# Optimization experiments

Measured on AMD Instinct MI355X. Metric: run time of the kernel, lower is better.

Reference implementation:

```python
import jax, jax.numpy as jnp
import numpy as np

C = 1024
H = 16
D = C // H  # head_dim = 64
FF = 4 * C


def setup_inputs() -> dict:
    key = jax.random.key(0)
    ks = jax.random.split(key, 10)
    s = lambda fan_in: 1.0 / np.sqrt(fan_in)
    return {
        "x": jax.random.normal(ks[0], (2, 2048, C), dtype=jnp.float32),
        "ln1_g": jnp.ones((C,), jnp.float32),
        "ln1_b": jnp.zeros((C,), jnp.float32),
        "w_qkv": jax.random.normal(ks[1], (C, 3 * C), jnp.float32) * s(C),
        "w_proj": jax.random.normal(ks[2], (C, C), jnp.float32) * s(C),
        "b_proj": jnp.zeros((C,), jnp.float32),
        "ln2_g": jnp.ones((C,), jnp.float32),
        "ln2_b": jnp.zeros((C,), jnp.float32),
        "w_fc1": jax.random.normal(ks[3], (C, FF), jnp.float32) * s(C),
        "b_fc1": jnp.zeros((FF,), jnp.float32),
        "w_fc2": jax.random.normal(ks[4], (FF, C), jnp.float32) * s(FF),
        "b_fc2": jnp.zeros((C,), jnp.float32),
    }


def _layernorm(x, g, b, eps=1e-5):
    mu = jnp.mean(x, axis=-1, keepdims=True)
    var = jnp.var(x, axis=-1, keepdims=True)
    return (x - mu) * jax.lax.rsqrt(var + eps) * g + b


def reference(x, ln1_g, ln1_b, w_qkv, w_proj, b_proj, ln2_g, ln2_b, w_fc1, b_fc1, w_fc2, b_fc2):
    B, N, _ = x.shape
    scale = D ** -0.5
    # --- attention sub-block (pre-LN) ---
    h = _layernorm(x, ln1_g, ln1_b)
    qkv = (h @ w_qkv).reshape(B, N, 3, H, D)
    q, k, v = jnp.moveaxis(qkv, 2, 0)          # each [B, N, H, D]
    attn = jnp.einsum("bnhd,bmhd->bhnm", q, k) * scale  # [B,H,N,N]
    attn = jax.nn.softmax(attn, axis=-1)
    o = jnp.einsum("bhnm,bmhd->bnhd", attn, v).reshape(B, N, C)
    x = x + o @ w_proj + b_proj
    # --- MLP sub-block (pre-LN) ---
    h = _layernorm(x, ln2_g, ln2_b)
    h = jax.nn.gelu(h @ w_fc1 + b_fc1, approximate=False)
    x = x + h @ w_fc2 + b_fc2
    return x
```

## Files before the change

kernel.cpp:

```cpp
#include <hip/hip_runtime.h>
#include <hip/hip_bf16.h>

typedef unsigned short u16;
typedef unsigned int u32;
typedef __attribute__((ext_vector_type(8))) short bf16x8;
typedef __attribute__((ext_vector_type(4))) float f32x4;
typedef __attribute__((ext_vector_type(4))) int   i32x4;
typedef __attribute__((ext_vector_type(4))) float fvec4;

__device__ inline u16 f2bf(float f) {
    union { float f; unsigned u; } v; v.f = f;
    unsigned r = v.u + 0x7fffu + ((v.u >> 16) & 1u);
    return (u16)(r >> 16);
}

__device__ inline f32x4 mfma16(bf16x8 a, bf16x8 b, f32x4 c) {
    return __builtin_amdgcn_mfma_f32_16x16x32_bf16(a, b, c, 0, 0, 0);
}

__device__ inline void gload16(const void* g, void* l) {
    __builtin_amdgcn_global_load_lds(
        (const __attribute__((address_space(1))) unsigned int*)g,
        (__attribute__((address_space(3))) unsigned int*)l, 16, 0, 0);
}

__global__ __launch_bounds__(256)
void transpose_all(const float* __restrict__ w0, u16* __restrict__ o0,
                   const float* __restrict__ w1, u16* __restrict__ o1,
                   const float* __restrict__ w2, u16* __restrict__ o2,
                   const float* __restrict__ w3, u16* __restrict__ o3) {
    __shared__ float tile[32][33];
    int b = blockIdx.x;
    const float* in; u16* out; int K, N, local;
    if (b < 3072)      { in = w0; out = o0; K = 1024; N = 3072; local = b; }
    else if (b < 4096) { in = w1; out = o1; K = 1024; N = 1024; local = b - 3072; }
    else if (b < 8192) { in = w2; out = o2; K = 1024; N = 4096; local = b - 4096; }
    else               { in = w3; out = o3; K = 4096; N = 1024; local = b - 8192; }
    const int nx = N >> 5;
    const int n0 = (local % nx) * 32, k0 = (local / nx) * 32;
    const int x = threadIdx.x & 31, y = threadIdx.x >> 5;
    for (int i = 0; i < 4; ++i)
        tile[y + i * 8][x] = in[(size_t)(k0 + y + i * 8) * N + n0 + x];
    __syncthreads();
    for (int i = 0; i < 4; ++i) {
        int r = y + i * 8;
        out[(size_t)(n0 + r) * K + k0 + x] = f2bf(tile[x][r]);
    }
}

__global__ __launch_bounds__(256)
void vtrans(const u16* __restrict__ qkv, u16* __restrict__ vT) {
    __shared__ u32 tl[64][33];
    const int t0 = blockIdx.x * 64, f0 = blockIdx.y * 64;
    const int a = threadIdx.x & 31, yy = threadIdx.x >> 5;
    for (int i = 0; i < 8; ++i) {
        int t = yy + i * 8;
        tl[t][a] = *(const u32*)(qkv + (size_t)(t0 + t) * 3072 + 2048 + f0 + a * 2);
    }
    __syncthreads();
    for (int i = 0; i < 8; ++i) {
        int f = yy + i * 8;
        u32 lo = tl[2 * a][f >> 1], hi = tl[2 * a + 1][f >> 1];
        u32 r = (f & 1) ? ((lo >> 16) | (hi & 0xffff0000u))
                        : ((lo & 0xffffu) | (hi << 16));
        *(u32*)(vT + (size_t)(f0 + f) * 4096 + t0 + 2 * a) = r;
    }
}

__global__ __launch_bounds__(256)
void ln_kernel(const float* __restrict__ x, const float* __restrict__ g,
               const float* __restrict__ bvec, u16* __restrict__ out) {
    __shared__ float red[2][4];
    const int row = blockIdx.x, tid = threadIdx.x;
    const float* xr = x + (size_t)row * 1024;
    fvec4 v = *(const fvec4*)(xr + tid * 4);
    float s  = v[0] + v[1] + v[2] + v[3];
    float s2 = v[0]*v[0] + v[1]*v[1] + v[2]*v[2] + v[3]*v[3];
    for (int off = 1; off < 64; off <<= 1) {
        s  += __shfl_xor(s,  off);
        s2 += __shfl_xor(s2, off);
    }
    const int w = tid >> 6;
    if ((tid & 63) == 0) { red[0][w] = s; red[1][w] = s2; }
    __syncthreads();
    s  = red[0][0] + red[0][1] + red[0][2] + red[0][3];
    s2 = red[1][0] + red[1][1] + red[1][2] + red[1][3];
    const float mu  = s * (1.0f / 1024.0f);
    const float var = s2 * (1.0f / 1024.0f) - mu * mu;
    const float rstd = rsqrtf(var + 1e-5f);
    fvec4 gv = *(const fvec4*)(g + tid * 4);
    fvec4 bv = *(const fvec4*)(bvec + tid * 4);
    u16 o4[4];
    for (int i = 0; i < 4; ++i)
        o4[i] = f2bf((v[i] - mu) * rstd * gv[i] + bv[i]);
    u32 lo = (u32)o4[0] | ((u32)o4[1] << 16);
    u32 hi = (u32)o4[2] | ((u32)o4[3] << 16);
    u32* dst = (u32*)(out + (size_t)row * 1024 + tid * 4);
    dst[0] = lo; dst[1] = hi;
}

template <int MODE, int WM, int WN, int MT, int NT, int NYP>
__global__ __launch_bounds__(256)
void gemm64(const u16* __restrict__ A, const u16* __restrict__ Bt,
            const float* __restrict__ bias, const float* __restrict__ res,
            void* __restrict__ out, int M, int N, int K) {
    constexpr int TM = WM * MT * 16;
    constexpr int TN = WN * NT * 16;
    constexpr int AJ = TM / 64;
    constexpr int BJ = TN / 64;
    static_assert(TM == 128, "swizzle assumes 32 M-tiles");
    __shared__ __attribute__((aligned(16))) u16 sA[2 * TM * 32];
    __shared__ __attribute__((aligned(16))) u16 sB[2 * TN * 32];
    const int id = blockIdx.x;
    const int j  = id >> 3;
    const int by = (id & 7) * NYP + (j >> 5);
    const int bx = j & 31;
    const int tid = threadIdx.x;
    const int lane = tid & 63, w = tid >> 6;
    const int wm = w / WN, wn = w % WN;
    const int q = lane >> 4, l16 = lane & 15;

    f32x4 acc[MT][NT];
#pragma unroll
    for (int i = 0; i < MT; ++i)
#pragma unroll
        for (int jj = 0; jj < NT; ++jj) acc[i][jj] = (f32x4)0.0f;

    const int sr = lane >> 2;
    const int kc = (lane & 3) * 8;
    const u16* gA[AJ];
    const u16* gB[BJ];
#pragma unroll
    for (int jj = 0; jj < AJ; ++jj)
        gA[jj] = A + (size_t)(bx * TM + (jj * 4 + w) * 16 + sr) * K + kc;
#pragma unroll
    for (int jj = 0; jj < BJ; ++jj)
        gB[jj] = Bt + (size_t)(by * TN + (jj * 4 + w) * 16 + sr) * K + kc;

    for (int k0 = 0; k0 < K; k0 += 64) {
#pragma unroll
        for (int kt = 0; kt < 2; ++kt) {
#pragma unroll
            for (int jj = 0; jj < AJ; ++jj)
                gload16(gA[jj] + k0 + kt * 32, &sA[kt * TM * 32 + (jj * 4 + w) * 512]);
#pragma unroll
            for (int jj = 0; jj < BJ; ++jj)
                gload16(gB[jj] + k0 + kt * 32, &sB[kt * TN * 32 + (jj * 4 + w) * 512]);
        }
        __syncthreads();
#pragma unroll
        for (int kt = 0; kt < 2; ++kt) {
            bf16x8 af[MT], bf[NT];
#pragma unroll
            for (int mt = 0; mt < MT; ++mt)
                af[mt] = *(const bf16x8*)&sA[kt * TM * 32 +
                         (wm * MT * 16 + mt * 16 + l16) * 32 + q * 8];
#pragma unroll
            for (int nt = 0; nt < NT; ++nt)
                bf[nt] = *(const bf16x8*)&sB[kt * TN * 32 +
                         (wn * NT * 16 + nt * 16 + l16) * 32 + q * 8];
#pragma unroll
            for (int mt = 0; mt < MT; ++mt)
#pragma unroll
                for (int nt = 0; nt < NT; ++nt)
                    acc[mt][nt] = mfma16(af[mt], bf[nt], acc[mt][nt]);
        }
        __syncthreads();
    }

#pragma unroll
    for (int mt = 0; mt < MT; ++mt)
#pragma unroll
        for (int nt = 0; nt < NT; ++nt)
#pragma unroll
            for (int r = 0; r < 4; ++r) {
                const int row = bx * TM + wm * MT * 16 + mt * 16 + q * 4 + r;
                const int col = by * TN + wn * NT * 16 + nt * 16 + l16;
                const size_t idx = (size_t)row * N + col;
                float v = acc[mt][nt][r];
                if (MODE == 0) {
                    ((u16*)out)[idx] = f2bf(v);
                } else if (MODE == 1) {
                    ((float*)out)[idx] = v + bias[col] + res[idx];
                } else {
                    float t = v + bias[col];
                    ((u16*)out)[idx] = f2bf(t * 0.5f * (1.0f + erff(t * 0.70710678118f)));
                }
            }
}

__global__ __launch_bounds__(256)
void attention3(const u16* __restrict__ qkv, const u16* __restrict__ vT,
                u16* __restrict__ o) {
    __shared__ __attribute__((aligned(16))) u16 sK[64][72];
    __shared__ __attribute__((aligned(16))) u16 sV[64][72];

    const int tid = threadIdx.x;
    const int lane = tid & 63, w = tid >> 6;
    const int qc = lane >> 4, l16 = lane & 15;
    const int bx = blockIdx.x;
    const int qt = bx & 15, h = (bx >> 4) & 15, b = bx >> 8;
    const int rowbase = qt * 128 + w * 32;

    bf16x8 aQ[2][2];
#pragma unroll
    for (int mtq = 0; mtq < 2; ++mtq)
#pragma unroll
        for (int kd = 0; kd < 2; ++kd)
            aQ[mtq][kd] = *(const bf16x8*)(qkv +
                (size_t)(b * 2048 + rowbase + mtq * 16 + l16) * 3072 +
                h * 64 + kd * 32 + qc * 8);

    f32x4 accO[2][4];
#pragma unroll
    for (int mtq = 0; mtq < 2; ++mtq)
#pragma unroll
        for (int dt = 0; dt < 4; ++dt) accO[mtq][dt] = (f32x4)0.0f;
    float lsum[2] = {0.0f, 0.0f};

    const int srr = tid >> 3;
    const int sc8 = (tid & 7) * 8;
    const u16* gK = qkv + (size_t)(b * 2048 + srr) * 3072 + 1024 + h * 64 + sc8;
    const u16* gV = vT + (size_t)(h * 64 + srr) * 4096 + b * 2048 + sc8;

    i32x4 cK[2], cV[2];
    cK[0] = *(const i32x4*)gK;
    cK[1] = *(const i32x4*)(gK + (size_t)32 * 3072);
    cV[0] = *(const i32x4*)gV;
    cV[1] = *(const i32x4*)(gV + (size_t)32 * 4096);

    const int sig_base = ((l16 >> 2) << 3) + (l16 & 3);

    for (int kc = 0; kc < 32; ++kc) {
        __syncthreads();
        *(i32x4*)&sK[srr][sc8]      = cK[0];
        *(i32x4*)&sK[srr + 32][sc8] = cK[1];
        *(i32x4*)&sV[srr][sc8]      = cV[0];
        *(i32x4*)&sV[srr + 32][sc8] = cV[1];
        const int kn = (kc + 1 < 32) ? kc + 1 : 31;
        i32x4 nK[2], nV[2];
        nK[0] = *(const i32x4*)(gK + (size_t)kn * 64 * 3072);
        nK[1] = *(const i32x4*)(gK + ((size_t)kn * 64 + 32) * 3072);
        nV[0] = *(const i32x4*)(gV + kn * 64);
        nV[1] = *(const i32x4*)(gV + (size_t)32 * 4096 + kn * 64);
        __syncthreads();

        bf16x8 kf[4][2];
#pragma unroll
        for (int mk = 0; mk < 4; ++mk) {
            const int krow = ((mk & 1) << 5) + ((mk >> 1) << 2) + sig_base;
            kf[mk][0] = *(const bf16x8*)&sK[krow][qc * 8];
            kf[mk][1] = *(const bf16x8*)&sK[krow][32 + qc * 8];
        }

        f32x4 s[2][4];
#pragma unroll
        for (int mtq = 0; mtq < 2; ++mtq)
#pragma unroll
            for (int mk = 0; mk < 4; ++mk) {
                f32x4 z = (f32x4)0.0f;
                z = mfma16(kf[mk][0], aQ[mtq][0], z);
                z = mfma16(kf[mk][1], aQ[mtq][1], z);
                s[mtq][mk] = z;
            }

        bf16x8 pf[2][2];
#pragma unroll
        for (int mtq = 0; mtq < 2; ++mtq) {
            float ls = 0.0f;
#pragma unroll
            for (int mk = 0; mk < 4; ++mk)
#pragma unroll
                for (int r = 0; r < 4; ++r) {
                    float p = __expf(s[mtq][mk][r] * 0.125f);
                    s[mtq][mk][r] = p;
                    ls += p;
                }
            lsum[mtq] += ls;
#pragma unroll
            for (int kt = 0; kt < 2; ++kt)
#pragma unroll
                for (int jj = 0; jj < 4; ++jj) {
                    pf[mtq][kt][jj]     = (short)f2bf(s[mtq][kt][jj]);
                    pf[mtq][kt][4 + jj] = (short)f2bf(s[mtq][2 + kt][jj]);
                }
        }

#pragma unroll
        for (int kt = 0; kt < 2; ++kt)
#pragma unroll
            for (int dt = 0; dt < 4; ++dt) {
                bf16x8 vf = *(const bf16x8*)&sV[dt * 16 + l16][kt * 32 + qc * 8];
#pragma unroll
                for (int mtq = 0; mtq < 2; ++mtq)
                    accO[mtq][dt] = mfma16(pf[mtq][kt], vf, accO[mtq][dt]);
            }

        cK[0] = nK[0]; cK[1] = nK[1];
        cV[0] = nV[0]; cV[1] = nV[1];
    }

#pragma unroll
    for (int mtq = 0; mtq < 2; ++mtq) {
        lsum[mtq] += __shfl_xor(lsum[mtq], 16);
        lsum[mtq] += __shfl_xor(lsum[mtq], 32);
    }

#pragma unroll
    for (int mtq = 0; mtq < 2; ++mtq)
#pragma unroll
        for (int r = 0; r < 4; ++r) {
            const float lr = __shfl(lsum[mtq], qc * 4 + r, 16);
            const float inv = 1.0f / lr;
            const size_t tok = (size_t)b * 2048 + rowbase + mtq * 16 + qc * 4 + r;
#pragma unroll
            for (int dt = 0; dt < 4; ++dt)
                o[tok * 1024 + h * 64 + dt * 16 + l16] = f2bf(accO[mtq][dt][r] * inv);
        }
}

extern "C" void kernel_launch(void* const* d_in, const int* in_sizes, int n_in,
                              void* d_out, int out_size, void* d_ws, size_t ws_size,
                              hipStream_t stream) {
    const float* x      = (const float*)d_in[0];
    const float* ln1_g  = (const float*)d_in[1];
    const float* ln1_b  = (const float*)d_in[2];
    const float* w_qkv  = (const float*)d_in[3];
    const float* w_proj = (const float*)d_in[4];
    const float* b_proj = (const float*)d_in[5];
    const float* ln2_g  = (const float*)d_in[6];
    const float* ln2_b  = (const float*)d_in[7];
    const float* w_fc1  = (const float*)d_in[8];
    const float* b_fc1  = (const float*)d_in[9];
    const float* w_fc2  = (const float*)d_in[10];
    const float* b_fc2  = (const float*)d_in[11];
    float* out = (float*)d_out;

    char* ws = (char*)d_ws;
    u16*   wqkvT  = (u16*)(ws + 0);
    u16*   wprojT = (u16*)(ws + 6291456);
    u16*   wfc1T  = (u16*)(ws + 8388608);
    u16*   wfc2T  = (u16*)(ws + 16777216);
    u16*   hA     = (u16*)(ws + 25165824);
    u16*   qkv    = (u16*)(ws + 33554432);
    float* x1     = (float*)(ws + 58720256);
    u16*   gbuf   = (u16*)(ws + 75497472);
    u16*   vT     = (u16*)(ws + 75497472);

    dim3 blk(256);
    transpose_all<<<12288, blk, 0, stream>>>(w_qkv, wqkvT, w_proj, wprojT,
                                             w_fc1, wfc1T, w_fc2, wfc2T);

    ln_kernel<<<4096, blk, 0, stream>>>(x, ln1_g, ln1_b, hA);
    gemm64<0, 2, 2, 4, 4, 3><<<768, blk, 0, stream>>>(hA, wqkvT, nullptr, nullptr, qkv, 4096, 3072, 1024);
    vtrans<<<dim3(64, 16), blk, 0, stream>>>(qkv, vT);
    attention3<<<512, blk, 0, stream>>>(qkv, vT, hA);
    gemm64<1, 4, 1, 2, 4, 2><<<512, blk, 0, stream>>>(hA, wprojT, b_proj, x, x1, 4096, 1024, 1024);

    u16* h2 = qkv;
    ln_kernel<<<4096, blk, 0, stream>>>(x1, ln2_g, ln2_b, h2);
    gemm64<2, 2, 2, 4, 4, 4><<<1024, blk, 0, stream>>>(h2, wfc1T, b_fc1, nullptr, gbuf, 4096, 4096, 1024);
    gemm64<1, 4, 1, 2, 4, 2><<<512, blk, 0, stream>>>(gbuf, wfc2T, b_fc2, x1, out, 4096, 1024, 4096);
}
```

Measured before the change: 366.6 us.

## Add 256x256-tile 8-wave GEMM with phased LDS pipeline for QKV and FC1

```diff
diff --git a/kernel.cpp b/kernel.cpp
--- a/kernel.cpp
+++ b/kernel.cpp
@@ -189,6 +189,120 @@
             }
 }
 
+template <int MODE>
+__global__ __launch_bounds__(512)
+void gemm256(const u16* __restrict__ A, const u16* __restrict__ Bt,
+             const float* __restrict__ bias, const float* __restrict__ res,
+             void* __restrict__ out, int M, int N, int K) {
+    __shared__ __attribute__((aligned(16))) u16 sA[2][16384];
+    __shared__ __attribute__((aligned(16))) u16 sB[2][16384];
+    const int tid  = threadIdx.x;
+    const int w    = tid >> 6, lane = tid & 63;
+    const int wm   = w >> 2,  wn   = w & 3;
+    const int q    = lane >> 4, l16 = lane & 15;
+    const int w8   = w << 3,  l8   = lane >> 3;
+    const int kch  = (lane & 7) ^ l8;
+
+    const int nwg  = gridDim.x;
+    const int id   = blockIdx.x;
+    const int wgid = (id & 7) * (nwg >> 3) + (id >> 3);
+    const int bx   = wgid & 15, by = wgid >> 4;
+
+    const u16* pAs = A  + (size_t)(bx * 256 + w8 + l8) * K + kch * 8;
+    const u16* pBs = Bt + (size_t)(by * 256 + w8 + l8) * K + kch * 8;
+
+    const int cs0  = ((q ^ (l16 & 7)) << 4);
+    const int cs1  = cs0 ^ 64;
+    const int aoff = (wm * 128 + l16) * 128;
+    const int boff = (wn * 64  + l16) * 128;
+
+    f32x4 acc[8][4];
+#pragma unroll
+    for (int m = 0; m < 8; ++m)
+#pragma unroll
+        for (int n = 0; n < 4; ++n) acc[m][n] = (f32x4)0.0f;
+
+#define GISS(P, r0, k0, SH, b_) \
+    gload16((P) + (size_t)((r0) * K + (k0)), &SH[b_][((r0) + w8) * 64])
+
+    GISS(pBs, 0, 0, sB, 0);  GISS(pBs, 64, 0, sB, 0);
+    GISS(pBs, 128, 0, sB, 0); GISS(pBs, 192, 0, sB, 0);
+    GISS(pAs, 0, 0, sA, 0);  GISS(pAs, 64, 0, sA, 0);
+    GISS(pAs, 128, 0, sA, 0); GISS(pAs, 192, 0, sA, 0);
+    GISS(pBs, 0, 64, sB, 1); GISS(pBs, 64, 64, sB, 1);
+    GISS(pBs, 128, 64, sB, 1); GISS(pBs, 192, 64, sB, 1);
+    asm volatile("s_waitcnt vmcnt(4)" ::: "memory");
+    __builtin_amdgcn_s_barrier();
+
+    bf16x8 bfr[4][2];
+
+#define PHASE(mq_, cb_, SP, SH, sb_, sr0, sk0) do {                          \
+    const char* bA_ = (const char*)&sA[cb_][0] + aoff;                       \
+    const char* bB_ = (const char*)&sB[cb_][0] + boff;                       \
+    if ((mq_) == 0) {                                                        \
+        _Pragma("unroll") for (int n = 0; n < 4; ++n) {                      \
+            bfr[n][0] = *(const bf16x8*)(bB_ + n * 2048 + cs0);              \
+            bfr[n][1] = *(const bf16x8*)(bB_ + n * 2048 + cs1);              \
+        }                                                                    \
+    }                                                                        \
+    bf16x8 af_[2][2];                                                        \
+    _Pragma("unroll") for (int mi = 0; mi < 2; ++mi) {                       \
+        af_[mi][0] = *(const bf16x8*)(bA_ + (2 * (mq_) + mi) * 2048 + cs0);  \
+        af_[mi][1] = *(const bf16x8*)(bA_ + (2 * (mq_) + mi) * 2048 + cs1);  \
+    }                                                                        \
+    GISS(SP, (sr0), (sk0), SH, sb_);                                         \
+    GISS(SP, (sr0) + 64, (sk0), SH, sb_);                                    \
+    __builtin_amdgcn_s_barrier();                                            \
+    __builtin_amdgcn_s_setprio(1);                                           \
+    _Pragma("unroll") for (int kt = 0; kt < 2; ++kt)                         \
+        _Pragma("unroll") for (int mi = 0; mi < 2; ++mi)                     \
+            _Pragma("unroll") for (int n = 0; n < 4; ++n)                    \
+                acc[2 * (mq_) + mi][n] =                                     \
+                    mfma16(af_[mi][kt], bfr[n][kt], acc[2 * (mq_) + mi][n]); \
+    __builtin_amdgcn_s_setprio(0);                                           \
+    if ((mq_) == 3) asm volatile("s_waitcnt vmcnt(4)" ::: "memory");         \
+    __builtin_amdgcn_s_barrier();                                            \
+} while (0)
+
+    const int NI = K >> 7;
+    for (int i = 0; i < NI; ++i) {
+        const int kb  = i << 7;
+        const int kA1 = kb + 64;
+        const int kN  = (kb + 128 < K) ? kb + 128 : K - 64;
+        const int kB1 = (kb + 192 < K) ? kb + 192 : K - 64;
+        PHASE(0, 0, pAs, sA, 1, 0,   kA1);
+        PHASE(1, 0, pAs, sA, 1, 128, kA1);
+        PHASE(2, 0, pBs, sB, 0, 0,   kN);
+        PHASE(3, 0, pBs, sB, 0, 128, kN);
+        PHASE(0, 1, pAs, sA, 0, 0,   kN);
+        PHASE(1, 1, pAs, sA, 0, 128, kN);
+        PHASE(2, 1, pBs, sB, 1, 0,   kB1);
+        PHASE(3, 1, pBs, sB, 1, 128, kB1);
+    }
+#undef PHASE
+#undef GISS
+
+#pragma unroll
+    for (int m = 0; m < 8; ++m)
+#pragma unroll
+        for (int n = 0; n < 4; ++n)
+#pragma unroll
+            for (int r = 0; r < 4; ++r) {
+                const int row = bx * 256 + wm * 128 + m * 16 + q * 4 + r;
+                const int col = by * 256 + wn * 64 + n * 16 + l16;
+                const size_t idx = (size_t)row * N + col;
+                float v = acc[m][n][r];
+                if (MODE == 0) {
+                    ((u16*)out)[idx] = f2bf(v);
+                } else if (MODE == 1) {
+                    ((float*)out)[idx] = v + bias[col] + res[idx];
+                } else {
+                    float t = v + bias[col];
+                    ((u16*)out)[idx] = f2bf(t * 0.5f * (1.0f + erff(t * 0.70710678118f)));
+                }
+            }
+}
+
 __global__ __launch_bounds__(256)
 void attention3(const u16* __restrict__ qkv, const u16* __restrict__ vT,
                 u16* __restrict__ o) {
@@ -352,13 +466,13 @@
                                              w_fc1, wfc1T, w_fc2, wfc2T);
 
     ln_kernel<<<4096, blk, 0, stream>>>(x, ln1_g, ln1_b, hA);
-    gemm64<0, 2, 2, 4, 4, 3><<<768, blk, 0, stream>>>(hA, wqkvT, nullptr, nullptr, qkv, 4096, 3072, 1024);
+    gemm256<0><<<192, dim3(512), 0, stream>>>(hA, wqkvT, nullptr, nullptr, qkv, 4096, 3072, 1024);
     vtrans<<<dim3(64, 16), blk, 0, stream>>>(qkv, vT);
     attention3<<<512, blk, 0, stream>>>(qkv, vT, hA);
     gemm64<1, 4, 1, 2, 4, 2><<<512, blk, 0, stream>>>(hA, wprojT, b_proj, x, x1, 4096, 1024, 1024);
 
     u16* h2 = qkv;
     ln_kernel<<<4096, blk, 0, stream>>>(x1, ln2_g, ln2_b, h2);
-    gemm64<2, 2, 2, 4, 4, 4><<<1024, blk, 0, stream>>>(h2, wfc1T, b_fc1, nullptr, gbuf, 4096, 4096, 1024);
+    gemm256<2><<<256, dim3(512), 0, stream>>>(h2, wfc1T, b_fc1, nullptr, gbuf, 4096, 4096, 1024);
     gemm64<1, 4, 1, 2, 4, 2><<<512, blk, 0, stream>>>(gbuf, wfc2T, b_fc2, x1, out, 4096, 1024, 4096);
 }
```

Result: no change. 361.5 us (-1.4%).
